# Kernel optimization log

Hardware: AMD Instinct MI355X
Metric: run time of the kernel (lower is better)

Reference implementation:

```python
import jax, jax.numpy as jnp
import numpy as np

HEADS = 8
DEPTH = 2
LN_EPS = 1e-5


def _layernorm(x, g, b):
    m = jnp.mean(x, axis=-1, keepdims=True)
    v = jnp.var(x, axis=-1, keepdims=True)
    return (x - m) / jnp.sqrt(v + LN_EPS) * g + b


def setup_inputs() -> dict:
    key = jax.random.key(0)
    ks = jax.random.split(key, 16)
    b, c, n, t = 4, 64, 512, 12
    L, H = DEPTH, 256  # depth, mlp_dim
    s = 0.05
    return {
        'x': jax.random.normal(ks[0], (b, c, n, t), jnp.float32),
        'adj': jax.random.uniform(ks[1], (n, n), jnp.float32) / n,
        'pos': 0.02 * jax.random.normal(ks[2], (1, n, c), jnp.float32),
        'qkv_w': s * jax.random.normal(ks[3], (L, 3 * c, c), jnp.float32),
        'proj_w': s * jax.random.normal(ks[4], (L, c, c), jnp.float32),
        'proj_b': jnp.zeros((L, c), jnp.float32),
        'ln_g': jnp.ones((L, c), jnp.float32),
        'ln_b': jnp.zeros((L, c), jnp.float32),
        'ff_w1': s * jax.random.normal(ks[5], (L, H, c), jnp.float32),
        'ff_b1': jnp.zeros((L, H), jnp.float32),
        'ff_w2': s * jax.random.normal(ks[6], (L, c, H), jnp.float32),
        'ff_b2': jnp.zeros((L, c), jnp.float32),
        'gcn_w': s * jax.random.normal(ks[7], (L, c, 3 * c), jnp.float32),  # Conv2d 1x1: [c_out, 3*c_in]
        'gcn_b': jnp.zeros((L, c), jnp.float32),
    }


def reference(x, adj, pos, qkv_w, proj_w, proj_b, ln_g, ln_b,
              ff_w1, ff_b1, ff_w2, ff_b2, gcn_w, gcn_b):
    b, c, n, t = x.shape
    hd = c // HEADS
    scale = hd ** (-0.5)
    # [b, c, n, t] -> [b*t, n, c]
    h = jnp.transpose(x, (0, 3, 2, 1)).reshape(b * t, n, c) + pos
    for l in range(DEPTH):
        residual = h.reshape(b, t, n, c)
        # --- manual MHA (no pre-norm around attention, faithful to source) ---
        qkv = jnp.einsum('bnc,oc->bno', h, qkv_w[l])  # [bt, n, 3c]
        qkv = qkv.reshape(b * t, n, 3, HEADS, hd).transpose(2, 0, 3, 1, 4)
        q, k, v = qkv[0], qkv[1], qkv[2]  # [bt, heads, n, hd]
        attn = jax.nn.softmax(jnp.einsum('bhnd,bhmd->bhnm', q, k) * scale, axis=-1)
        o = jnp.einsum('bhnm,bhmd->bhnd', attn, v)
        o = o.transpose(0, 2, 1, 3).reshape(b * t, n, c)
        o = jnp.einsum('bnc,oc->bno', o, proj_w[l]) + proj_b[l]
        h = o + h
        # --- PreNorm FeedForward ---
        y = _layernorm(h, ln_g[l], ln_b[l])
        y = jax.nn.gelu(jnp.einsum('bnc,hc->bnh', y, ff_w1[l]) + ff_b1[l], approximate=False)
        y = jnp.einsum('bnh,ch->bnc', y, ff_w2[l]) + ff_b2[l]
        h = y + h
        # --- GCN on residual (order=2 diffusion) ---
        r = jnp.transpose(residual, (0, 3, 2, 1))  # [b, c, n, t]
        x1 = jnp.einsum('bcvt,vw->bcwt', r, adj)
        x2 = jnp.einsum('bcvt,vw->bcwt', x1, adj)
        cat = jnp.concatenate([r, x1, x2], axis=1)  # [b, 3c, n, t]
        g = jnp.einsum('bknt,ok->bont', cat, gcn_w[l]) + gcn_b[l][None, :, None, None]
        h = jnp.transpose(g, (0, 3, 2, 1)).reshape(b * t, n, c) + h
    return jnp.transpose(h.reshape(b, t, n, c), (0, 3, 2, 1))
```

## Files before the change

### kernel.cpp

```cpp
#include <hip/hip_runtime.h>
#include <math.h>


typedef __fp16 half_t;
typedef __attribute__((ext_vector_type(2))) __fp16 half2v;
typedef __attribute__((ext_vector_type(4))) __fp16 half4v;
typedef __attribute__((ext_vector_type(4))) float f32x4;

union PU  { half2v h2[2]; half4v h4; };
union F4H { float4 f; half4v h[2]; };
union F2H { float2 f2; half4v h4; };

#define ATS 72
#define BTS 68
#define KLS 20
#define QLS 20
#define VTS 516

__global__ __launch_bounds__(256) void k_pre(const float* __restrict__ x,
                                             const float* __restrict__ pos,
                                             const float* __restrict__ adj,
                                             const float* __restrict__ qkv_w,
                                             const float* __restrict__ proj_w,
                                             const float* __restrict__ ff_w1,
                                             const float* __restrict__ ff_w2,
                                             const float* __restrict__ gcn_w,
                                             float* __restrict__ h,
                                             half_t* __restrict__ adjTh,
                                             half_t* __restrict__ wh) {
    __shared__ float t[64 * 65];
    int tid = threadIdx.x;
    int bidx = blockIdx.x;
    if (bidx < 384) {
        int b = bidx / 96, vt0 = (bidx % 96) * 64;
#pragma unroll
        for (int i = 0; i < 4; ++i) {
            int g = tid + i * 256;
            int r = g >> 4, q = g & 15;
            *(float4*)&t[r * 65 + 4 * q] =
                *(const float4*)(x + ((size_t)(b * 64 + r)) * 6144 + vt0 + 4 * q);
        }
        __syncthreads();
#pragma unroll
        for (int i = 0; i < 4; ++i) {
            int g = tid + i * 256;
            int r = g >> 4, q = g & 15;
            int vt = vt0 + r;
            int v = vt / 12, tt = vt - v * 12;
            float4 pv = *(const float4*)(pos + v * 64 + 4 * q);
            float4 o;
            o.x = t[(4 * q + 0) * 65 + r] + pv.x;
            o.y = t[(4 * q + 1) * 65 + r] + pv.y;
            o.z = t[(4 * q + 2) * 65 + r] + pv.z;
            o.w = t[(4 * q + 3) * 65 + r] + pv.w;
            *(float4*)(h + ((size_t)((b * 12 + tt) * 512 + v)) * 64 + 4 * q) = o;
        }
    } else if (bidx < 448) {
        int fb = bidx - 384;
        int v0 = (fb & 7) * 64, w0 = (fb >> 3) * 64;
#pragma unroll
        for (int i = 0; i < 4; ++i) {
            int g = tid + i * 256;
            int r = g >> 4, q = g & 15;
            float4 a = *(const float4*)(adj + (size_t)(v0 + r) * 512 + w0 + 4 * q);
            t[(4 * q + 0) * 65 + r] = a.x;
            t[(4 * q + 1) * 65 + r] = a.y;
            t[(4 * q + 2) * 65 + r] = a.z;
            t[(4 * q + 3) * 65 + r] = a.w;
        }
        __syncthreads();
#pragma unroll
        for (int i = 0; i < 4; ++i) {
            int g = tid + i * 256;
            int rw = g >> 4, q = g & 15;
            const float* src = &t[rw * 65 + 4 * q];
            PU u;
            u.h2[0] = __builtin_amdgcn_cvt_pkrtz(src[0], src[1]);
            u.h2[1] = __builtin_amdgcn_cvt_pkrtz(src[2], src[3]);
            *(half4v*)(adjTh + (size_t)(w0 + rw) * 512 + v0 + 4 * q) = u.h4;
        }
    } else {
        int i = (bidx - 448) * 256 + tid;
        float v;
        if (i < 24576) v = qkv_w[i];
        else if (i < 32768) v = proj_w[i - 24576];
        else if (i < 65536) v = ff_w1[i - 32768];
        else if (i < 98304) v = ff_w2[i - 65536];
        else v = gcn_w[i - 98304];
        wh[i] = (half_t)v;
    }
}

__global__ __launch_bounds__(256) void k_adj2(const half_t* __restrict__ adjTh,
                                              half_t* __restrict__ adjT2h) {
    __shared__ half_t a_t[64 * ATS];
    __shared__ half_t b_t[64 * BTS];
    int tid = threadIdx.x;
    int wave = tid >> 6, lane = tid & 63;
    int lm = lane & 15, lg = lane >> 4;
    int w0 = blockIdx.x * 64, v0 = blockIdx.y * 64;
    const f32x4 zc = {0.f, 0.f, 0.f, 0.f};
    f32x4 acc[4] = {zc, zc, zc, zc};

    for (int kc = 0; kc < 8; ++kc) {
#pragma unroll
        for (int i = 0; i < 2; ++i) {
            int g = tid + i * 256;
            int r = g >> 3, s = g & 7;
            *(float4*)&a_t[r * ATS + s * 8] =
                *(const float4*)(adjTh + (size_t)(w0 + r) * 512 + kc * 64 + s * 8);
        }
#pragma unroll
        for (int i = 0; i < 2; ++i) {
            int g = tid + i * 256;
            int ur = g >> 3, s = g & 7;
            F4H u;
            u.f = *(const float4*)(adjTh + (size_t)(kc * 64 + ur) * 512 + v0 + s * 8);
#pragma unroll
            for (int e = 0; e < 8; ++e)
                b_t[(s * 8 + e) * BTS + ur] = u.h[e >> 2][e & 3];
        }
        __syncthreads();
#pragma unroll
        for (int k16 = 0; k16 < 4; ++k16) {
            half4v af = *(const half4v*)&a_t[(wave * 16 + lm) * ATS + k16 * 16 + lg * 4];
#pragma unroll
            for (int nt = 0; nt < 4; ++nt) {
                half4v bf = *(const half4v*)&b_t[(nt * 16 + lm) * BTS + k16 * 16 + lg * 4];
                acc[nt] = __builtin_amdgcn_mfma_f32_16x16x16f16(af, bf, acc[nt], 0, 0, 0);
            }
        }
        __syncthreads();
    }
#pragma unroll
    for (int nt = 0; nt < 4; ++nt)
#pragma unroll
        for (int r = 0; r < 4; ++r)
            adjT2h[(size_t)(w0 + wave * 16 + lg * 4 + r) * 512 + v0 + nt * 16 + lm] =
                (half_t)acc[nt][r];
}

__global__ __launch_bounds__(256) void k_qd(const float* __restrict__ h,
                                            const half_t* __restrict__ Wh,
                                            half_t* __restrict__ qh,
                                            half_t* __restrict__ kh,
                                            half_t* __restrict__ vh,
                                            const half_t* __restrict__ adjTh,
                                            const half_t* __restrict__ adjT2h,
                                            half_t* __restrict__ x1h,
                                            half_t* __restrict__ x2h) {
    __shared__ __align__(16) half_t sbuf[64 * ATS + 64 * BTS];
    int tid = threadIdx.x;
    int bidx = blockIdx.x;
    int wave = tid >> 6, lane = tid & 63;
    int lm = lane & 15, lg = lane >> 4;
    const f32x4 zc = {0.f, 0.f, 0.f, 0.f};

    if (bidx < 384) {
        int wid = bidx * 4 + wave;
        int row = wid * 16 + lm;
        half4v xf[4];
#pragma unroll
        for (int kc = 0; kc < 4; ++kc) {
            float4 a = *(const float4*)(h + (size_t)row * 64 + kc * 16 + lg * 4);
            PU u;
            u.h2[0] = __builtin_amdgcn_cvt_pkrtz(a.x, a.y);
            u.h2[1] = __builtin_amdgcn_cvt_pkrtz(a.z, a.w);
            xf[kc] = u.h4;
        }
        const float SC = 0.35355339059327373f * 1.4426950408889634f;
        int bt = row >> 9, v = row & 511;
        half4v wf[4];
#pragma unroll
        for (int kc = 0; kc < 4; ++kc)
            wf[kc] = *(const half4v*)(Wh + (size_t)lm * 64 + kc * 16 + lg * 4);
#pragma unroll
        for (int nt = 0; nt < 12; ++nt) {
            half4v cw[4];
#pragma unroll
            for (int kc = 0; kc < 4; ++kc) cw[kc] = wf[kc];
            if (nt < 11) {
#pragma unroll
                for (int kc = 0; kc < 4; ++kc)
                    wf[kc] = *(const half4v*)(Wh + (size_t)((nt + 1) * 16 + lm) * 64 + kc * 16 + lg * 4);
            }
            f32x4 acc = zc;
#pragma unroll
            for (int kc = 0; kc < 4; ++kc)
                acc = __builtin_amdgcn_mfma_f32_16x16x16f16(cw[kc], xf[kc], acc, 0, 0, 0);
            int s = nt >> 2;
            if (s == 0) { acc[0] *= SC; acc[1] *= SC; acc[2] *= SC; acc[3] *= SC; }
            int head = ((nt & 3) << 1) + (lg >> 1);
            int d0 = (lg & 1) * 4;
            PU o2;
            o2.h2[0] = __builtin_amdgcn_cvt_pkrtz(acc[0], acc[1]);
            o2.h2[1] = __builtin_amdgcn_cvt_pkrtz(acc[2], acc[3]);
            half_t* dst = (s == 0) ? qh : ((s == 1) ? kh : vh);
            *(half4v*)(dst + ((size_t)(bt * 8 + head) * 512 + v) * 8 + d0) = o2.h4;
        }
    } else {
        half_t* a_t = sbuf;
        half_t* b_t = sbuf + 64 * ATS;
        int fb = bidx - 384;
        int z = fb / 384, rem = fb - z * 384;
        int w0 = (rem & 7) * 64;
        int bt = rem >> 3;
        const half_t* A = z ? adjT2h : adjTh;
        half_t* outb = z ? x2h : x1h;
        f32x4 acc[4] = {zc, zc, zc, zc};
        for (int kc = 0; kc < 8; ++kc) {
#pragma unroll
            for (int i = 0; i < 2; ++i) {
                int g = tid + i * 256;
                int r = g >> 3, s = g & 7;
                *(float4*)&a_t[r * ATS + s * 8] =
                    *(const float4*)(A + (size_t)(w0 + r) * 512 + kc * 64 + s * 8);
            }
#pragma unroll
            for (int i = 0; i < 4; ++i) {
                int g = tid + i * 256;
                int vr = g >> 4, q = g & 15;
                float4 a = *(const float4*)(h + ((size_t)(bt * 512 + kc * 64 + vr)) * 64 + 4 * q);
                b_t[(4 * q + 0) * BTS + vr] = (half_t)a.x;
                b_t[(4 * q + 1) * BTS + vr] = (half_t)a.y;
                b_t[(4 * q + 2) * BTS + vr] = (half_t)a.z;
                b_t[(4 * q + 3) * BTS + vr] = (half_t)a.w;
            }
            __syncthreads();
#pragma unroll
            for (int k16 = 0; k16 < 4; ++k16) {
                half4v af = *(const half4v*)&a_t[(wave * 16 + lm) * ATS + k16 * 16 + lg * 4];
#pragma unroll
                for (int nt = 0; nt < 4; ++nt) {
                    half4v bf = *(const half4v*)&b_t[(nt * 16 + lm) * BTS + k16 * 16 + lg * 4];
                    acc[nt] = __builtin_amdgcn_mfma_f32_16x16x16f16(af, bf, acc[nt], 0, 0, 0);
                }
            }
            __syncthreads();
        }
#pragma unroll
        for (int nt = 0; nt < 4; ++nt)
#pragma unroll
            for (int r = 0; r < 4; ++r)
                outb[(size_t)(w0 + wave * 16 + lg * 4 + r) * 3072 + bt * 64 + nt * 16 + lm] =
                    (half_t)acc[nt][r];
    }
}

__global__ __launch_bounds__(512) void k_ag(const half_t* __restrict__ qh,
                                            const half_t* __restrict__ kh,
                                            const half_t* __restrict__ vh,
                                            half_t* __restrict__ obh,
                                            const float* __restrict__ h,
                                            const half_t* __restrict__ x1h,
                                            const half_t* __restrict__ x2h,
                                            const half_t* __restrict__ Wh,
                                            const float* __restrict__ bias,
                                            float* __restrict__ gout) {
    __shared__ __align__(16) half_t sbuf[512 * KLS + 16 * VTS + 256 * QLS];
    int tid = threadIdx.x;
    int bidx = blockIdx.x;
    const half4v zero4 = {(__fp16)0.f, (__fp16)0.f, (__fp16)0.f, (__fp16)0.f};
    const f32x4 zc = {0.f, 0.f, 0.f, 0.f};

    if (bidx < 768) {
        half_t* kl = sbuf;
        half_t* vt = sbuf + 512 * KLS;
        half_t* ql = sbuf + 512 * KLS + 16 * VTS;
        int bh = bidx >> 1;
        int half_ = bidx & 1;
        const half_t* kbase = kh + (size_t)bh * 4096;
        const half_t* vbase = vh + (size_t)bh * 4096;
        const half_t* qbase = qh + (size_t)bh * 4096 + half_ * 2048;

        if (tid < 256) {
#pragma unroll
            for (int kk = 0; kk < 2; ++kk) {
                int key = tid * 2 + kk;
                F4H u;
                u.f = *(const float4*)(kbase + key * 8);
                half4v* rowp = (half4v*)&kl[key * KLS];
                rowp[0] = u.h[0];
                rowp[1] = u.h[1];
                rowp[2] = zero4;
                rowp[3] = zero4;
            }
            {
                F4H u;
                u.f = *(const float4*)(qbase + tid * 8);
                half4v* rowp = (half4v*)&ql[tid * QLS];
                rowp[0] = u.h[0];
                rowp[1] = u.h[1];
                rowp[2] = zero4;
                rowp[3] = zero4;
            }
            {
                int k0 = tid * 2;
                F4H a, b;
                a.f = *(const float4*)(vbase + k0 * 8);
                b.f = *(const float4*)(vbase + k0 * 8 + 8);
#pragma unroll
                for (int d = 0; d < 8; ++d) {
                    half2v p = {a.h[d >> 2][d & 3], b.h[d >> 2][d & 3]};
                    *(half2v*)&vt[d * VTS + k0] = p;
                }
            }
        }
        for (int i = tid; i < 1032; i += 512)
            ((half4v*)(vt + 8 * VTS))[i] = zero4;
        __syncthreads();

        int wave = tid >> 6, lane = tid & 63;
        int lm = lane & 15, lg = lane >> 4;
        int bt = bh >> 3, head = bh & 7;

#pragma unroll 1
        for (int st = 0; st < 2; ++st) {
            int qrow0 = wave * 32 + st * 16;
            half4v qf = *(const half4v*)&ql[(qrow0 + lm) * QLS + lg * 4];
            f32x4 acc = zc;
            float l0 = 0.f, l1 = 0.f, l2 = 0.f, l3 = 0.f;
#pragma unroll 4
            for (int kt = 0; kt < 32; ++kt) {
                int key0 = kt * 16;
                half4v ka = *(const half4v*)&kl[(key0 + lm) * KLS + lg * 4];
                f32x4 c1 = __builtin_amdgcn_mfma_f32_16x16x16f16(ka, qf, zc, 0, 0, 0);
                float p0 = exp2f(fminf(c1[0], 12.f));
                float p1 = exp2f(fminf(c1[1], 12.f));
                float p2 = exp2f(fminf(c1[2], 12.f));
                float p3 = exp2f(fminf(c1[3], 12.f));
                l0 += p0; l1 += p1; l2 += p2; l3 += p3;
                PU pu;
                pu.h2[0] = __builtin_amdgcn_cvt_pkrtz(p0, p1);
                pu.h2[1] = __builtin_amdgcn_cvt_pkrtz(p2, p3);
                half4v va = *(const half4v*)&vt[lm * VTS + key0 + lg * 4];
                acc = __builtin_amdgcn_mfma_f32_16x16x16f16(va, pu.h4, acc, 0, 0, 0);
            }
            float lsum = (l0 + l1) + (l2 + l3);
            lsum += __shfl_xor(lsum, 16);
            lsum += __shfl_xor(lsum, 32);
            if (lg < 2) {
                float inv = 1.f / lsum;
                int rowg = half_ * 256 + qrow0 + lm;
                PU o2;
                o2.h2[0] = __builtin_amdgcn_cvt_pkrtz(acc[0] * inv, acc[1] * inv);
                o2.h2[1] = __builtin_amdgcn_cvt_pkrtz(acc[2] * inv, acc[3] * inv);
                *(half4v*)(obh + ((size_t)(bt * 512 + rowg)) * 64 + head * 8 + lg * 4) = o2.h4;
            }
        }
    } else {
        half_t* a_t = sbuf;
        half_t* b_t = sbuf + 64 * ATS;
        int row0 = (bidx - 768) * 64;
        int wave = tid >> 6, lane = tid & 63;
        int lm = lane & 15, lg = lane >> 4;
        f32x4 acc[4] = {zc, zc, zc, zc};

        for (int ch = 0; ch < 3; ++ch) {
            if (tid < 256) {
                if (ch == 0) {
#pragma unroll
                    for (int i = 0; i < 4; ++i) {
                        int g = tid + i * 256;
                        int r = g >> 4, q = g & 15;
                        int rowg = row0 + r;
                        int v = rowg / 48, bt = rowg - v * 48;
                        float4 a = *(const float4*)(h + ((size_t)(bt * 512 + v)) * 64 + 4 * q);
                        PU ua;
                        ua.h2[0] = __builtin_amdgcn_cvt_pkrtz(a.x, a.y);
                        ua.h2[1] = __builtin_amdgcn_cvt_pkrtz(a.z, a.w);
                        *(half4v*)&a_t[r * ATS + 4 * q] = ua.h4;
                    }
                } else {
                    const half_t* X = (ch == 1) ? x1h : x2h;
#pragma unroll
                    for (int i = 0; i < 2; ++i) {
                        int g = tid + i * 256;
                        int r = g >> 3, s = g & 7;
                        *(float4*)&a_t[r * ATS + s * 8] =
                            *(const float4*)(X + (size_t)(row0 + r) * 64 + s * 8);
                    }
                }
#pragma unroll
                for (int i = 0; i < 4; ++i) {
                    int g = tid + i * 256;
                    int r = g >> 4, q = g & 15;
                    *(half4v*)&b_t[r * BTS + 4 * q] =
                        *(const half4v*)(Wh + (size_t)r * 192 + ch * 64 + 4 * q);
                }
            }
            __syncthreads();
            if (tid < 256) {
#pragma unroll
                for (int k16 = 0; k16 < 4; ++k16) {
                    half4v af = *(const half4v*)&a_t[(wave * 16 + lm) * ATS + k16 * 16 + lg * 4];
#pragma unroll
                    for (int nt = 0; nt < 4; ++nt) {
                        half4v bf = *(const half4v*)&b_t[(nt * 16 + lm) * BTS + k16 * 16 + lg * 4];
                        acc[nt] = __builtin_amdgcn_mfma_f32_16x16x16f16(bf, af, acc[nt], 0, 0, 0);
                    }
                }
            }
            __syncthreads();
        }
        if (tid < 256) {
            int row = row0 + wave * 16 + lm;
            int v = row / 48, bt = row - v * 48;
            float* gp = gout + ((size_t)(bt * 512 + v)) * 64;
#pragma unroll
            for (int nt = 0; nt < 4; ++nt) {
                float4 bb = *(const float4*)(bias + nt * 16 + lg * 4);
                *(float4*)(gp + nt * 16 + lg * 4) =
                    make_float4(acc[nt][0] + bb.x, acc[nt][1] + bb.y,
                                acc[nt][2] + bb.z, acc[nt][3] + bb.w);
            }
        }
    }
}

__global__ __launch_bounds__(128) void k_plf(const half_t* __restrict__ obh,
                                             const half_t* __restrict__ pwh,
                                             const float* __restrict__ pb,
                                             const float* __restrict__ g,
                                             const float* __restrict__ bln,
                                             const half_t* __restrict__ w1h,
                                             const float* __restrict__ b1,
                                             const half_t* __restrict__ w2h,
                                             const float* __restrict__ b2,
                                             const float* __restrict__ gout,
                                             float* __restrict__ h) {
    int wid = blockIdx.x * 2 + (threadIdx.x >> 6);
    int lane = threadIdx.x & 63;
    int lm = lane & 15, lg = lane >> 4;
    int row = wid * 16 + lm;
    const f32x4 zc = {0.f, 0.f, 0.f, 0.f};

    half4v pf[4];
#pragma unroll
    for (int kc = 0; kc < 4; ++kc)
        pf[kc] = *(const half4v*)(pwh + (size_t)lm * 64 + kc * 16 + lg * 4);

    half4v of[4];
#pragma unroll
    for (int kc = 0; kc < 4; ++kc) {
        F2H u;
        u.f2 = *(const float2*)(obh + (size_t)row * 64 + kc * 16 + lg * 4);
        of[kc] = u.h4;
    }

    f32x4 hp[4];
#pragma unroll
    for (int nt = 0; nt < 4; ++nt) {
        half4v cw[4];
#pragma unroll
        for (int kc = 0; kc < 4; ++kc) cw[kc] = pf[kc];
        if (nt < 3) {
#pragma unroll
            for (int kc = 0; kc < 4; ++kc)
                pf[kc] = *(const half4v*)(pwh + (size_t)((nt + 1) * 16 + lm) * 64 + kc * 16 + lg * 4);
        }
        f32x4 c = zc;
#pragma unroll
        for (int kc = 0; kc < 4; ++kc)
            c = __builtin_amdgcn_mfma_f32_16x16x16f16(cw[kc], of[kc], c, 0, 0, 0);
        float4 ho = *(const float4*)(h + (size_t)row * 64 + nt * 16 + lg * 4);
        float4 bb = *(const float4*)(pb + nt * 16 + lg * 4);
        hp[nt][0] = c[0] + ho.x + bb.x;
        hp[nt][1] = c[1] + ho.y + bb.y;
        hp[nt][2] = c[2] + ho.z + bb.z;
        hp[nt][3] = c[3] + ho.w + bb.w;
    }

    float s = 0.f, s2 = 0.f;
#pragma unroll
    for (int nt = 0; nt < 4; ++nt)
#pragma unroll
        for (int r = 0; r < 4; ++r) {
            s += hp[nt][r];
            s2 += hp[nt][r] * hp[nt][r];
        }
    s += __shfl_xor(s, 16);  s2 += __shfl_xor(s2, 16);
    s += __shfl_xor(s, 32);  s2 += __shfl_xor(s2, 32);
    float mean = s * (1.f / 64.f);
    float var = s2 * (1.f / 64.f) - mean * mean;
    float rstd = rsqrtf(var + 1e-5f);

    half4v xf[4];
#pragma unroll
    for (int nt = 0; nt < 4; ++nt) {
        float4 gg = *(const float4*)(g + nt * 16 + lg * 4);
        float4 bb = *(const float4*)(bln + nt * 16 + lg * 4);
        float y0 = (hp[nt][0] - mean) * rstd * gg.x + bb.x;
        float y1 = (hp[nt][1] - mean) * rstd * gg.y + bb.y;
        float y2 = (hp[nt][2] - mean) * rstd * gg.z + bb.z;
        float y3 = (hp[nt][3] - mean) * rstd * gg.w + bb.w;
        PU u;
        u.h2[0] = __builtin_amdgcn_cvt_pkrtz(y0, y1);
        u.h2[1] = __builtin_amdgcn_cvt_pkrtz(y2, y3);
        xf[nt] = u.h4;
    }

    half4v w1f[4];
#pragma unroll
    for (int kc = 0; kc < 4; ++kc)
        w1f[kc] = *(const half4v*)(w1h + (size_t)lm * 64 + kc * 16 + lg * 4);

    f32x4 acc[4] = {zc, zc, zc, zc};
#pragma unroll 4
    for (int ht = 0; ht < 16; ++ht) {
        half4v cw[4];
#pragma unroll
        for (int kc = 0; kc < 4; ++kc) cw[kc] = w1f[kc];
        half4v w2f[4];
#pragma unroll
        for (int ot = 0; ot < 4; ++ot)
            w2f[ot] = *(const half4v*)(w2h + (size_t)(ot * 16 + lm) * 256 + ht * 16 + lg * 4);
        if (ht < 15) {
#pragma unroll
            for (int kc = 0; kc < 4; ++kc)
                w1f[kc] = *(const half4v*)(w1h + (size_t)((ht + 1) * 16 + lm) * 64 + kc * 16 + lg * 4);
        }
        f32x4 c1 = zc;
#pragma unroll
        for (int kc = 0; kc < 4; ++kc)
            c1 = __builtin_amdgcn_mfma_f32_16x16x16f16(cw[kc], xf[kc], c1, 0, 0, 0);
        float4 bb = *(const float4*)(b1 + ht * 16 + lg * 4);
        float y0 = c1[0] + bb.x;
        float y1 = c1[1] + bb.y;
        float y2 = c1[2] + bb.z;
        float y3 = c1[3] + bb.w;
        y0 = 0.5f * y0 * (1.0f + erff(y0 * 0.70710678118654752f));
        y1 = 0.5f * y1 * (1.0f + erff(y1 * 0.70710678118654752f));
        y2 = 0.5f * y2 * (1.0f + erff(y2 * 0.70710678118654752f));
        y3 = 0.5f * y3 * (1.0f + erff(y3 * 0.70710678118654752f));
        PU p;
        p.h2[0] = __builtin_amdgcn_cvt_pkrtz(y0, y1);
        p.h2[1] = __builtin_amdgcn_cvt_pkrtz(y2, y3);
#pragma unroll
        for (int ot = 0; ot < 4; ++ot)
            acc[ot] = __builtin_amdgcn_mfma_f32_16x16x16f16(w2f[ot], p.h4, acc[ot], 0, 0, 0);
    }

#pragma unroll
    for (int ot = 0; ot < 4; ++ot) {
        float4 bb = *(const float4*)(b2 + ot * 16 + lg * 4);
        float4 gv = *(const float4*)(gout + (size_t)row * 64 + ot * 16 + lg * 4);
        *(float4*)(h + (size_t)row * 64 + ot * 16 + lg * 4) =
            make_float4(hp[ot][0] + acc[ot][0] + bb.x + gv.x,
                        hp[ot][1] + acc[ot][1] + bb.y + gv.y,
                        hp[ot][2] + acc[ot][2] + bb.z + gv.z,
                        hp[ot][3] + acc[ot][3] + bb.w + gv.w);
    }
}

__global__ __launch_bounds__(256) void k_out(const float* __restrict__ h,
                                             float* __restrict__ out) {
    __shared__ float t[64 * 65];
    int tid = threadIdx.x;
    int b = blockIdx.x / 96, vt0 = (blockIdx.x % 96) * 64;
#pragma unroll
    for (int i = 0; i < 4; ++i) {
        int g = tid + i * 256;
        int r = g >> 4, q = g & 15;
        int vt = vt0 + r;
        int v = vt / 12, tt = vt - v * 12;
        *(float4*)&t[r * 65 + 4 * q] =
            *(const float4*)(h + ((size_t)((b * 12 + tt) * 512 + v)) * 64 + 4 * q);
    }
    __syncthreads();
#pragma unroll
    for (int i = 0; i < 4; ++i) {
        int g = tid + i * 256;
        int r = g >> 4, q = g & 15;
        float4 o;
        o.x = t[(4 * q + 0) * 65 + r];
        o.y = t[(4 * q + 1) * 65 + r];
        o.z = t[(4 * q + 2) * 65 + r];
        o.w = t[(4 * q + 3) * 65 + r];
        *(float4*)(out + ((size_t)(b * 64 + r)) * 6144 + vt0 + 4 * q) = o;
    }
}

extern "C" void kernel_launch(void* const* d_in, const int* in_sizes, int n_in,
                              void* d_out, int out_size, void* d_ws, size_t ws_size,
                              hipStream_t stream) {
    const float* x      = (const float*)d_in[0];
    const float* adj    = (const float*)d_in[1];
    const float* pos    = (const float*)d_in[2];
    const float* qkv_w  = (const float*)d_in[3];
    const float* proj_w = (const float*)d_in[4];
    const float* proj_b = (const float*)d_in[5];
    const float* ln_g   = (const float*)d_in[6];
    const float* ln_b   = (const float*)d_in[7];
    const float* ff_w1  = (const float*)d_in[8];
    const float* ff_b1  = (const float*)d_in[9];
    const float* ff_w2  = (const float*)d_in[10];
    const float* ff_b2  = (const float*)d_in[11];
    const float* gcn_w  = (const float*)d_in[12];
    const float* gcn_b  = (const float*)d_in[13];
    float* out = (float*)d_out;

    const size_t SZ = 1572864;
    float* h    = (float*)d_ws;
    float* gout = h + SZ;
    half_t* x1h = (half_t*)(gout + SZ);
    half_t* x2h = x1h + SZ;
    half_t* qh  = x2h + SZ;
    half_t* kh  = qh + SZ;
    half_t* vh  = kh + SZ;
    half_t* obh = vh + SZ;
    half_t* adjTh  = obh + SZ;
    half_t* adjT2h = adjTh + 262144;
    half_t* wh     = adjT2h + 262144;
    half_t* qkv_wh  = wh;
    half_t* proj_wh = wh + 24576;
    half_t* ff_w1h  = wh + 32768;
    half_t* ff_w2h  = wh + 65536;
    half_t* gcn_wh  = wh + 98304;

    k_pre<<<928, 256, 0, stream>>>(x, pos, adj, qkv_w, proj_w, ff_w1, ff_w2, gcn_w,
                                   h, adjTh, wh);
    k_adj2<<<dim3(8, 8), 256, 0, stream>>>(adjTh, adjT2h);
    for (int l = 0; l < 2; ++l) {
        k_qd<<<1152, 256, 0, stream>>>(h, qkv_wh + l * 12288, qh, kh, vh,
                                       adjTh, adjT2h, x1h, x2h);
        k_ag<<<1152, 512, 0, stream>>>(qh, kh, vh, obh, h, x1h, x2h,
                                       gcn_wh + l * 12288, gcn_b + l * 64, gout);
        k_plf<<<768, 128, 0, stream>>>(obh, proj_wh + l * 4096, proj_b + l * 64,
                                       ln_g + l * 64, ln_b + l * 64,
                                       ff_w1h + l * 16384, ff_b1 + l * 256,
                                       ff_w2h + l * 16384, ff_b2 + l * 64, gout, h);
    }
    k_out<<<384, 256, 0, stream>>>(h, out);
}
```

Before: 288.0 us.

## Keep fp16 shadow of hidden state and fuse both adjacency diffusion GEMMs per block

The producers of h (k_pre and k_plf) now also write an fp16 copy, so k_qd and k_ag read half the bytes and skip the per-load fp32-to-fp16 conversion. The k_qd diffusion branch also computes x1 and x2 in the same block from one shared staging of h. This halves its block count and removes the duplicate loads of h tiles. In exchange there are extra fp16 stores, a larger LDS footprint and more accumulators per thread.

```diff
diff --git a/kernel.cpp b/kernel.cpp
--- a/kernel.cpp
+++ b/kernel.cpp
@@ -26,6 +26,7 @@
                                              const float* __restrict__ ff_w2,
                                              const float* __restrict__ gcn_w,
                                              float* __restrict__ h,
+                                             half_t* __restrict__ hh,
                                              half_t* __restrict__ adjTh,
                                              half_t* __restrict__ wh) {
     __shared__ float t[64 * 65];
@@ -53,7 +54,12 @@
             o.y = t[(4 * q + 1) * 65 + r] + pv.y;
             o.z = t[(4 * q + 2) * 65 + r] + pv.z;
             o.w = t[(4 * q + 3) * 65 + r] + pv.w;
-            *(float4*)(h + ((size_t)((b * 12 + tt) * 512 + v)) * 64 + 4 * q) = o;
+            size_t idx = ((size_t)((b * 12 + tt) * 512 + v)) * 64 + 4 * q;
+            *(float4*)(h + idx) = o;
+            PU u;
+            u.h2[0] = __builtin_amdgcn_cvt_pkrtz(o.x, o.y);
+            u.h2[1] = __builtin_amdgcn_cvt_pkrtz(o.z, o.w);
+            *(half4v*)(hh + idx) = u.h4;
         }
     } else if (bidx < 448) {
         int fb = bidx - 384;
@@ -140,7 +146,7 @@
                 (half_t)acc[nt][r];
 }
 
-__global__ __launch_bounds__(256) void k_qd(const float* __restrict__ h,
+__global__ __launch_bounds__(256) void k_qd(const half_t* __restrict__ hh,
                                             const half_t* __restrict__ Wh,
                                             half_t* __restrict__ qh,
                                             half_t* __restrict__ kh,
@@ -149,7 +155,7 @@
                                             const half_t* __restrict__ adjT2h,
                                             half_t* __restrict__ x1h,
                                             half_t* __restrict__ x2h) {
-    __shared__ __align__(16) half_t sbuf[64 * ATS + 64 * BTS];
+    __shared__ __align__(16) half_t sbuf[2 * 64 * ATS + 64 * BTS];
     int tid = threadIdx.x;
     int bidx = blockIdx.x;
     int wave = tid >> 6, lane = tid & 63;
@@ -162,10 +168,8 @@
         half4v xf[4];
 #pragma unroll
         for (int kc = 0; kc < 4; ++kc) {
-            float4 a = *(const float4*)(h + (size_t)row * 64 + kc * 16 + lg * 4);
-            PU u;
-            u.h2[0] = __builtin_amdgcn_cvt_pkrtz(a.x, a.y);
-            u.h2[1] = __builtin_amdgcn_cvt_pkrtz(a.z, a.w);
+            F2H u;
+            u.f2 = *(const float2*)(hh + (size_t)row * 64 + kc * 16 + lg * 4);
             xf[kc] = u.h4;
         }
         const float SC = 0.35355339059327373f * 1.4426950408889634f;
@@ -199,41 +203,49 @@
             *(half4v*)(dst + ((size_t)(bt * 8 + head) * 512 + v) * 8 + d0) = o2.h4;
         }
     } else {
-        half_t* a_t = sbuf;
-        half_t* b_t = sbuf + 64 * ATS;
+        half_t* a_t  = sbuf;
+        half_t* a2_t = sbuf + 64 * ATS;
+        half_t* b_t  = sbuf + 2 * 64 * ATS;
         int fb = bidx - 384;
-        int z = fb / 384, rem = fb - z * 384;
-        int w0 = (rem & 7) * 64;
-        int bt = rem >> 3;
-        const half_t* A = z ? adjT2h : adjTh;
-        half_t* outb = z ? x2h : x1h;
-        f32x4 acc[4] = {zc, zc, zc, zc};
+        int w0 = (fb & 7) * 64;
+        int bt = fb >> 3;
+        f32x4 acc0[4] = {zc, zc, zc, zc};
+        f32x4 acc1[4] = {zc, zc, zc, zc};
         for (int kc = 0; kc < 8; ++kc) {
+#pragma unroll
+            for (int i = 0; i < 4; ++i) {
+                int g = tid + i * 256;
+                if (g < 512) {
+                    int r = g >> 3, s = g & 7;
+                    *(float4*)&a_t[r * ATS + s * 8] =
+                        *(const float4*)(adjTh + (size_t)(w0 + r) * 512 + kc * 64 + s * 8);
+                } else {
+                    int g2 = g - 512;
+                    int r = g2 >> 3, s = g2 & 7;
+                    *(float4*)&a2_t[r * ATS + s * 8] =
+                        *(const float4*)(adjT2h + (size_t)(w0 + r) * 512 + kc * 64 + s * 8);
+                }
+            }
 #pragma unroll
             for (int i = 0; i < 2; ++i) {
                 int g = tid + i * 256;
-                int r = g >> 3, s = g & 7;
-                *(float4*)&a_t[r * ATS + s * 8] =
-                    *(const float4*)(A + (size_t)(w0 + r) * 512 + kc * 64 + s * 8);
-            }
-#pragma unroll
-            for (int i = 0; i < 4; ++i) {
-                int g = tid + i * 256;
-                int vr = g >> 4, q = g & 15;
-                float4 a = *(const float4*)(h + ((size_t)(bt * 512 + kc * 64 + vr)) * 64 + 4 * q);
-                b_t[(4 * q + 0) * BTS + vr] = (half_t)a.x;
-                b_t[(4 * q + 1) * BTS + vr] = (half_t)a.y;
-                b_t[(4 * q + 2) * BTS + vr] = (half_t)a.z;
-                b_t[(4 * q + 3) * BTS + vr] = (half_t)a.w;
+                int vr = g >> 3, s = g & 7;
+                F4H u;
+                u.f = *(const float4*)(hh + ((size_t)(bt * 512 + kc * 64 + vr)) * 64 + s * 8);
+#pragma unroll
+                for (int e = 0; e < 8; ++e)
+                    b_t[(s * 8 + e) * BTS + vr] = u.h[e >> 2][e & 3];
             }
             __syncthreads();
 #pragma unroll
             for (int k16 = 0; k16 < 4; ++k16) {
-                half4v af = *(const half4v*)&a_t[(wave * 16 + lm) * ATS + k16 * 16 + lg * 4];
+                half4v af0 = *(const half4v*)&a_t[(wave * 16 + lm) * ATS + k16 * 16 + lg * 4];
+                half4v af1 = *(const half4v*)&a2_t[(wave * 16 + lm) * ATS + k16 * 16 + lg * 4];
 #pragma unroll
                 for (int nt = 0; nt < 4; ++nt) {
                     half4v bf = *(const half4v*)&b_t[(nt * 16 + lm) * BTS + k16 * 16 + lg * 4];
-                    acc[nt] = __builtin_amdgcn_mfma_f32_16x16x16f16(af, bf, acc[nt], 0, 0, 0);
+                    acc0[nt] = __builtin_amdgcn_mfma_f32_16x16x16f16(af0, bf, acc0[nt], 0, 0, 0);
+                    acc1[nt] = __builtin_amdgcn_mfma_f32_16x16x16f16(af1, bf, acc1[nt], 0, 0, 0);
                 }
             }
             __syncthreads();
@@ -241,9 +253,11 @@
 #pragma unroll
         for (int nt = 0; nt < 4; ++nt)
 #pragma unroll
-            for (int r = 0; r < 4; ++r)
-                outb[(size_t)(w0 + wave * 16 + lg * 4 + r) * 3072 + bt * 64 + nt * 16 + lm] =
-                    (half_t)acc[nt][r];
+            for (int r = 0; r < 4; ++r) {
+                size_t o = (size_t)(w0 + wave * 16 + lg * 4 + r) * 3072 + bt * 64 + nt * 16 + lm;
+                x1h[o] = (half_t)acc0[nt][r];
+                x2h[o] = (half_t)acc1[nt][r];
+            }
     }
 }
 
@@ -251,7 +265,7 @@
                                             const half_t* __restrict__ kh,
                                             const half_t* __restrict__ vh,
                                             half_t* __restrict__ obh,
-                                            const float* __restrict__ h,
+                                            const half_t* __restrict__ hh,
                                             const half_t* __restrict__ x1h,
                                             const half_t* __restrict__ x2h,
                                             const half_t* __restrict__ Wh,
@@ -360,16 +374,13 @@
             if (tid < 256) {
                 if (ch == 0) {
 #pragma unroll
-                    for (int i = 0; i < 4; ++i) {
+                    for (int i = 0; i < 2; ++i) {
                         int g = tid + i * 256;
-                        int r = g >> 4, q = g & 15;
+                        int r = g >> 3, s = g & 7;
                         int rowg = row0 + r;
                         int v = rowg / 48, bt = rowg - v * 48;
-                        float4 a = *(const float4*)(h + ((size_t)(bt * 512 + v)) * 64 + 4 * q);
-                        PU ua;
-                        ua.h2[0] = __builtin_amdgcn_cvt_pkrtz(a.x, a.y);
-                        ua.h2[1] = __builtin_amdgcn_cvt_pkrtz(a.z, a.w);
-                        *(half4v*)&a_t[r * ATS + 4 * q] = ua.h4;
+                        *(float4*)&a_t[r * ATS + s * 8] =
+                            *(const float4*)(hh + ((size_t)(bt * 512 + v)) * 64 + s * 8);
                     }
                 } else {
                     const half_t* X = (ch == 1) ? x1h : x2h;
@@ -428,7 +439,8 @@
                                              const half_t* __restrict__ w2h,
                                              const float* __restrict__ b2,
                                              const float* __restrict__ gout,
-                                             float* __restrict__ h) {
+                                             float* __restrict__ h,
+                                             half_t* __restrict__ hh) {
     int wid = blockIdx.x * 2 + (threadIdx.x >> 6);
     int lane = threadIdx.x & 63;
     int lm = lane & 15, lg = lane >> 4;
@@ -545,11 +557,16 @@
     for (int ot = 0; ot < 4; ++ot) {
         float4 bb = *(const float4*)(b2 + ot * 16 + lg * 4);
         float4 gv = *(const float4*)(gout + (size_t)row * 64 + ot * 16 + lg * 4);
-        *(float4*)(h + (size_t)row * 64 + ot * 16 + lg * 4) =
-            make_float4(hp[ot][0] + acc[ot][0] + bb.x + gv.x,
-                        hp[ot][1] + acc[ot][1] + bb.y + gv.y,
-                        hp[ot][2] + acc[ot][2] + bb.z + gv.z,
-                        hp[ot][3] + acc[ot][3] + bb.w + gv.w);
+        float4 fv = make_float4(hp[ot][0] + acc[ot][0] + bb.x + gv.x,
+                                hp[ot][1] + acc[ot][1] + bb.y + gv.y,
+                                hp[ot][2] + acc[ot][2] + bb.z + gv.z,
+                                hp[ot][3] + acc[ot][3] + bb.w + gv.w);
+        size_t idx = (size_t)row * 64 + ot * 16 + lg * 4;
+        *(float4*)(h + idx) = fv;
+        PU u;
+        u.h2[0] = __builtin_amdgcn_cvt_pkrtz(fv.x, fv.y);
+        u.h2[1] = __builtin_amdgcn_cvt_pkrtz(fv.z, fv.w);
+        *(half4v*)(hh + idx) = u.h4;
     }
 }
 
@@ -603,7 +620,8 @@
     const size_t SZ = 1572864;
     float* h    = (float*)d_ws;
     float* gout = h + SZ;
-    half_t* x1h = (half_t*)(gout + SZ);
+    half_t* hh  = (half_t*)(gout + SZ);
+    half_t* x1h = hh + SZ;
     half_t* x2h = x1h + SZ;
     half_t* qh  = x2h + SZ;
     half_t* kh  = qh + SZ;
@@ -619,17 +637,17 @@
     half_t* gcn_wh  = wh + 98304;
 
     k_pre<<<928, 256, 0, stream>>>(x, pos, adj, qkv_w, proj_w, ff_w1, ff_w2, gcn_w,
-                                   h, adjTh, wh);
+                                   h, hh, adjTh, wh);
     k_adj2<<<dim3(8, 8), 256, 0, stream>>>(adjTh, adjT2h);
     for (int l = 0; l < 2; ++l) {
-        k_qd<<<1152, 256, 0, stream>>>(h, qkv_wh + l * 12288, qh, kh, vh,
-                                       adjTh, adjT2h, x1h, x2h);
-        k_ag<<<1152, 512, 0, stream>>>(qh, kh, vh, obh, h, x1h, x2h,
+        k_qd<<<768, 256, 0, stream>>>(hh, qkv_wh + l * 12288, qh, kh, vh,
+                                      adjTh, adjT2h, x1h, x2h);
+        k_ag<<<1152, 512, 0, stream>>>(qh, kh, vh, obh, hh, x1h, x2h,
                                        gcn_wh + l * 12288, gcn_b + l * 64, gout);
         k_plf<<<768, 128, 0, stream>>>(obh, proj_wh + l * 4096, proj_b + l * 64,
                                        ln_g + l * 64, ln_b + l * 64,
                                        ff_w1h + l * 16384, ff_b1 + l * 256,
-                                       ff_w2h + l * 16384, ff_b2 + l * 64, gout, h);
+                                       ff_w2h + l * 16384, ff_b2 + l * 64, gout, h, hh);
     }
     k_out<<<384, 256, 0, stream>>>(h, out);
 }
```

Result: faster. 280.3 us (-2.7%).
